# Performance work log

Measured on AMD Instinct MI355X. Metric: run time of the kernel, lower is better.

Reference implementation:

```python
import jax, jax.numpy as jnp
import numpy as np

DT = 0.001
TAU_MEM = 0.01
TAU_SYN = 0.005
THRESHOLD = 1.0
INITIAL_STATE = 0.0
SS_BETA = 100.0  # SuperSpike surrogate slope (Zenke & Ganguli)


@jax.custom_vjp
def superspike(x):
    # Heaviside spike in forward
    return (x > 0).astype(x.dtype)

def _ss_fwd(x):
    return superspike(x), x

def _ss_bwd(x, g):
    # fast-sigmoid surrogate gradient
    return (g / (SS_BETA * jnp.abs(x) + 1.0) ** 2,)

superspike.defvjp(_ss_fwd, _ss_bwd)


def setup_inputs() -> dict:
    key = jax.random.key(0)
    k1, k2 = jax.random.split(key)
    B, T, IN, OUT = 64, 1024, 256, 256
    inputs = jax.random.normal(k1, (B, T, IN), dtype=jnp.float32)
    w = jax.random.normal(k2, (IN, OUT), dtype=jnp.float32) * 4.0  # scale=4.0 in __init__
    return {"inputs": inputs, "w": w}


def _simulate_mem(inputs, w):
    # inputs: [B, T, IN], w: [IN, OUT]
    x = jnp.matmul(inputs, w)  # [B, T, OUT]
    T = x.shape[1]
    dcy_mem = jnp.exp(jnp.asarray(-DT / (TAU_MEM + 1e-16), dtype=x.dtype))
    scl_mem = 1.0 - dcy_mem
    dcy_syn = jnp.exp(jnp.asarray(-DT / (TAU_SYN + 1e-16), dtype=x.dtype))

    zeros0 = jnp.zeros_like(x[:, 0])  # initial_state = 0

    def step(carry, x_t):
        syn, mem = carry
        new_syn = dcy_syn * syn + x_t
        new_mem = dcy_mem * mem + scl_mem * syn  # uses OLD syn
        out = superspike(mem - THRESHOLD)        # spike from OLD mem
        new_mem = new_mem * (1.0 - out)          # reset
        return (new_syn, new_mem), new_mem

    # loop runs over t = 0 .. T-2 (matches `for t in range(nb_steps - 1)`)
    xs = jnp.swapaxes(x[:, : T - 1], 0, 1)  # [T-1, B, OUT]
    _, mems = jax.lax.scan(step, (zeros0, zeros0), xs)
    mems = jnp.swapaxes(mems, 0, 1)  # [B, T-1, OUT]
    # prepend the initial stored state (zeros, since initial_state=0)
    U = jnp.concatenate([zeros0[:, None, :], mems], axis=1)  # [B, T, OUT]
    return U


def reference(inputs, w):
    # monitor == 'mem' -> return membrane potential trace U
    return _simulate_mem(inputs, w)
```

## Files before the change

kernel.cpp:

```cpp
#include <hip/hip_runtime.h>
#include <cmath>

typedef short bf16x8 __attribute__((ext_vector_type(8)));
typedef float f32x4 __attribute__((ext_vector_type(4)));
typedef unsigned short us8v __attribute__((ext_vector_type(8)));

#define T_DIM 1024

__device__ __forceinline__ unsigned short rtn_bf16(float f) {
    unsigned u = __float_as_uint(f);
    return (unsigned short)((u + 0x7FFFu + ((u >> 16) & 1u)) >> 16);
}
__device__ __forceinline__ float bf_to_f(unsigned short h) {
    return __uint_as_float(((unsigned)h) << 16);
}
__device__ __forceinline__ void split3(float f, unsigned short& h1,
                                       unsigned short& h2, unsigned short& h3) {
    unsigned u = __float_as_uint(f);
    h1 = (unsigned short)(u >> 16);
    float r1 = f - __uint_as_float(u & 0xFFFF0000u);
    unsigned u1 = __float_as_uint(r1);
    h2 = (unsigned short)(u1 >> 16);
    float r2 = r1 - __uint_as_float(u1 & 0xFFFF0000u);
    h3 = rtn_bf16(r2);
}

__device__ __forceinline__ void split_store8(const float4& a, const float4& b,
                                             unsigned short* __restrict__ A0,
                                             unsigned short* __restrict__ A1,
                                             unsigned short* __restrict__ A2,
                                             int off) {
    const float fv[8] = {a.x, a.y, a.z, a.w, b.x, b.y, b.z, b.w};
    us8v o1, o2, o3;
    #pragma unroll
    for (int i = 0; i < 8; ++i) {
        unsigned short h1, h2, h3;
        split3(fv[i], h1, h2, h3);
        o1[i] = h1; o2[i] = h2; o3[i] = h3;
    }
    *(us8v*)&A0[off] = o1;
    *(us8v*)&A1[off] = o2;
    *(us8v*)&A2[off] = o3;
}

__global__ __launch_bounds__(256) void lif_wsplit(const float* __restrict__ w,
                                                  unsigned short* __restrict__ wT1,
                                                  unsigned short* __restrict__ wT2,
                                                  unsigned short* __restrict__ wT3) {
    const int id = blockIdx.x * 256 + threadIdx.x;
    const int k = id >> 8, n = id & 255;
    unsigned short h1, h2, h3;
    split3(w[id], h1, h2, h3);
    const int o = n * 256 + k;
    wT1[o] = h1; wT2[o] = h2; wT3[o] = h3;
}

__global__ __launch_bounds__(256) void lif_gemm_mfma(const float* __restrict__ in,
                                                     const unsigned short* __restrict__ wT1,
                                                     const unsigned short* __restrict__ wT2,
                                                     const unsigned short* __restrict__ wT3,
                                                     float* __restrict__ xbuf) {
    __shared__ unsigned short As[2][3][128 * 32];

    const int tid  = threadIdx.x;
    const int bm   = blockIdx.x;
    const int bn   = blockIdx.y;
    const int wave = tid >> 6;
    const int lane = tid & 63;
    const int l15  = lane & 15;
    const int quad = lane >> 4;
    const int wm   = (wave >> 1) * 64;
    const int wn   = (wave & 1) * 64;

    f32x4 acc[4][4];
    #pragma unroll
    for (int i = 0; i < 4; ++i)
        #pragma unroll
        for (int j = 0; j < 4; ++j) acc[i][j] = (f32x4){0.f, 0.f, 0.f, 0.f};

    const int r  = tid >> 1;
    const int hf = tid & 1;
    const int rx = r & 3;
    const int off0 = r * 32 + (((hf << 1) | 0) ^ rx) * 8;
    const int off1 = r * 32 + (((hf << 1) | 1) ^ rx) * 8;
    const float* arow = in + (size_t)(bm * 128 + r) * 256 + hf * 16;

    float4 av0[4];
    #pragma unroll
    for (int j = 0; j < 4; ++j) av0[j] = *(const float4*)(arow + j * 4);
    float4 avn[4];
    #pragma unroll
    for (int j = 0; j < 4; ++j) avn[j] = *(const float4*)(arow + 32 + j * 4);
    split_store8(av0[0], av0[1], &As[0][0][0], &As[0][1][0], &As[0][2][0], off0);
    split_store8(av0[2], av0[3], &As[0][0][0], &As[0][1][0], &As[0][2][0], off1);
    __syncthreads();

    #pragma unroll
    for (int kt = 0; kt < 8; ++kt) {
        const int cur = kt & 1;

        bf16x8 af[3][4];
        #pragma unroll
        for (int mt = 0; mt < 4; ++mt) {
            const int m  = wm + mt * 16 + l15;
            const int ro = m * 32 + ((quad ^ (m & 3)) * 8);
            af[0][mt] = *(const bf16x8*)&As[cur][0][ro];
            af[1][mt] = *(const bf16x8*)&As[cur][1][ro];
            af[2][mt] = *(const bf16x8*)&As[cur][2][ro];
        }

        if (kt < 7) {
            split_store8(avn[0], avn[1], &As[cur ^ 1][0][0], &As[cur ^ 1][1][0],
                         &As[cur ^ 1][2][0], off0);
            split_store8(avn[2], avn[3], &As[cur ^ 1][0][0], &As[cur ^ 1][1][0],
                         &As[cur ^ 1][2][0], off1);
        }

        __syncthreads();

        if (kt < 6) {
            const float* ap = arow + (kt + 2) * 32;
            #pragma unroll
            for (int j = 0; j < 4; ++j) avn[j] = *(const float4*)(ap + j * 4);
        }

        const int k0 = kt * 32;
        size_t wo = (size_t)(bn * 128 + wn + l15) * 256 + k0 + quad * 8;
        bf16x8 b1 = *(const bf16x8*)(wT1 + wo);
        bf16x8 b2 = *(const bf16x8*)(wT2 + wo);
        bf16x8 b3 = *(const bf16x8*)(wT3 + wo);

        #pragma unroll
        for (int nt = 0; nt < 4; ++nt) {
            bf16x8 n1, n2, n3;
            if (nt < 3) {
                const size_t won = wo + (size_t)16 * 256;
                n1 = *(const bf16x8*)(wT1 + won);
                n2 = *(const bf16x8*)(wT2 + won);
                n3 = *(const bf16x8*)(wT3 + won);
            }
            #pragma unroll
            for (int mt = 0; mt < 4; ++mt) {
                f32x4 a = acc[mt][nt];
                a = __builtin_amdgcn_mfma_f32_16x16x32_bf16(af[0][mt], b1, a, 0, 0, 0);
                a = __builtin_amdgcn_mfma_f32_16x16x32_bf16(af[0][mt], b2, a, 0, 0, 0);
                a = __builtin_amdgcn_mfma_f32_16x16x32_bf16(af[1][mt], b1, a, 0, 0, 0);
                a = __builtin_amdgcn_mfma_f32_16x16x32_bf16(af[1][mt], b2, a, 0, 0, 0);
                a = __builtin_amdgcn_mfma_f32_16x16x32_bf16(af[0][mt], b3, a, 0, 0, 0);
                a = __builtin_amdgcn_mfma_f32_16x16x32_bf16(af[2][mt], b1, a, 0, 0, 0);
                acc[mt][nt] = a;
            }
            if (nt < 3) { b1 = n1; b2 = n2; b3 = n3; wo += (size_t)16 * 256; }
        }
    }

    #pragma unroll
    for (int mt = 0; mt < 4; ++mt) {
        #pragma unroll
        for (int nt = 0; nt < 4; ++nt) {
            const int C  = bn * 128 + wn + nt * 16 + l15;
            const int Rb = bm * 128 + wm + mt * 16 + quad * 4;
            #pragma unroll
            for (int reg = 0; reg < 4; ++reg)
                xbuf[(size_t)(Rb + reg) * 256 + C] = acc[mt][nt][reg];
        }
    }
}

__global__ __launch_bounds__(64, 1) void lif_scan(const float* __restrict__ xbuf,
                                                  float* __restrict__ U,
                                                  double dcy_syn, double dcy_mem,
                                                  double scl_mem) {
    const int b = blockIdx.x >> 2;
    const int o = (blockIdx.x & 3) * 64 + threadIdx.x;

    const float* xp = xbuf + (size_t)b * T_DIM * 256 + o;
    float* up = U + (size_t)b * T_DIM * 256 + o;

    up[0] = 0.0f;
    double syn = 0.0, mem = 0.0;

    float bufA[64], bufB[64];
    #pragma unroll
    for (int j = 0; j < 64; ++j)
        bufA[j] = __builtin_nontemporal_load(xp + (size_t)j * 256);

    #pragma unroll 1
    for (int bt = 0; bt < 8; ++bt) {
        const int tb = bt * 128;
        {
            const float* np = xp + (size_t)(tb + 64) * 256;
            #pragma unroll
            for (int j = 0; j < 64; ++j)
                bufB[j] = __builtin_nontemporal_load(np + (size_t)j * 256);
        }
        #pragma unroll
        for (int j = 0; j < 64; ++j) {
            const int t = tb + j;
            double nm = dcy_mem * mem + scl_mem * syn;
            if (mem - 1.0 > 0.0) nm = 0.0;
            syn = dcy_syn * syn + (double)bufA[j];
            mem = nm;
            __builtin_nontemporal_store((float)mem, up + (size_t)(t + 1) * 256);
        }
        if (bt < 7) {
            const float* np = xp + (size_t)(tb + 128) * 256;
            #pragma unroll
            for (int j = 0; j < 64; ++j)
                bufA[j] = __builtin_nontemporal_load(np + (size_t)j * 256);
        }
        #pragma unroll
        for (int j = 0; j < 64; ++j) {
            const int t = tb + 64 + j;
            double nm = dcy_mem * mem + scl_mem * syn;
            if (mem - 1.0 > 0.0) nm = 0.0;
            syn = dcy_syn * syn + (double)bufB[j];
            mem = nm;
            if (t < T_DIM - 1)
                __builtin_nontemporal_store((float)mem, up + (size_t)(t + 1) * 256);
        }
    }
}

extern "C" void kernel_launch(void* const* d_in, const int* in_sizes, int n_in,
                              void* d_out, int out_size, void* d_ws, size_t ws_size,
                              hipStream_t stream) {
    const float* in = (const float*)d_in[0];
    const float* w  = (const float*)d_in[1];
    float* U = (float*)d_out;

    const double dcy_mem = exp(-0.001 / (0.01  + 1e-16));
    const double dcy_syn = exp(-0.001 / (0.005 + 1e-16));
    const double scl_mem = 1.0 - dcy_mem;

    char* ws = (char*)d_ws;
    unsigned short* wT1 = (unsigned short*)ws;
    unsigned short* wT2 = (unsigned short*)(ws + 131072);
    unsigned short* wT3 = (unsigned short*)(ws + 262144);
    float* xbuf = (float*)(ws + 524288);

    lif_wsplit<<<dim3(256), dim3(256), 0, stream>>>(w, wT1, wT2, wT3);
    lif_gemm_mfma<<<dim3(512, 2), dim3(256), 0, stream>>>(in, wT1, wT2, wT3, xbuf);
    lif_scan<<<dim3(256), dim3(64), 0, stream>>>(xbuf, U, dcy_syn, dcy_mem, scl_mem);
}
```

Before: 189.6 us.

## Interleave LDS staging and B prefetch across MFMA loop; plain loads in scan

The GEMM main loop now spreads the split-and-store of the next A tile and the global prefetch across the inner nt iterations, so they overlap with MFMA work. The first B fragment of the next k-tile is prefetched at the end of the current one, and there is one barrier per k-step, at its end. Launch bounds now ask for 3 blocks per CU, which caps registers. The scan kernel switches its xbuf reads from nontemporal to ordinary loads, which may allow cache hits on data the GEMM just wrote. The tighter register cap risks spills.

New measurement: 226.2 us. 19.3% more time.

```diff
diff --git a/kernel.cpp b/kernel.cpp
--- a/kernel.cpp
+++ b/kernel.cpp
@@ -55,11 +55,11 @@
     wT1[o] = h1; wT2[o] = h2; wT3[o] = h3;
 }
 
-__global__ __launch_bounds__(256) void lif_gemm_mfma(const float* __restrict__ in,
-                                                     const unsigned short* __restrict__ wT1,
-                                                     const unsigned short* __restrict__ wT2,
-                                                     const unsigned short* __restrict__ wT3,
-                                                     float* __restrict__ xbuf) {
+__global__ __launch_bounds__(256, 3) void lif_gemm_mfma(const float* __restrict__ in,
+                                                        const unsigned short* __restrict__ wT1,
+                                                        const unsigned short* __restrict__ wT2,
+                                                        const unsigned short* __restrict__ wT3,
+                                                        float* __restrict__ xbuf) {
     __shared__ unsigned short As[2][3][128 * 32];
 
     const int tid  = threadIdx.x;
@@ -85,6 +85,8 @@
     const int off1 = r * 32 + (((hf << 1) | 1) ^ rx) * 8;
     const float* arow = in + (size_t)(bm * 128 + r) * 256 + hf * 16;
 
+    const size_t wrow = (size_t)(bn * 128 + wn + l15) * 256 + quad * 8;
+
     float4 av0[4];
     #pragma unroll
     for (int j = 0; j < 4; ++j) av0[j] = *(const float4*)(arow + j * 4);
@@ -94,6 +96,10 @@
     split_store8(av0[0], av0[1], &As[0][0][0], &As[0][1][0], &As[0][2][0], off0);
     split_store8(av0[2], av0[3], &As[0][0][0], &As[0][1][0], &As[0][2][0], off1);
     __syncthreads();
+
+    bf16x8 b1 = *(const bf16x8*)(wT1 + wrow);
+    bf16x8 b2 = *(const bf16x8*)(wT2 + wrow);
+    bf16x8 b3 = *(const bf16x8*)(wT3 + wrow);
 
     #pragma unroll
     for (int kt = 0; kt < 8; ++kt) {
@@ -109,32 +115,13 @@
             af[2][mt] = *(const bf16x8*)&As[cur][2][ro];
         }
 
-        if (kt < 7) {
-            split_store8(avn[0], avn[1], &As[cur ^ 1][0][0], &As[cur ^ 1][1][0],
-                         &As[cur ^ 1][2][0], off0);
-            split_store8(avn[2], avn[3], &As[cur ^ 1][0][0], &As[cur ^ 1][1][0],
-                         &As[cur ^ 1][2][0], off1);
-        }
-
-        __syncthreads();
-
-        if (kt < 6) {
-            const float* ap = arow + (kt + 2) * 32;
-            #pragma unroll
-            for (int j = 0; j < 4; ++j) avn[j] = *(const float4*)(ap + j * 4);
-        }
-
-        const int k0 = kt * 32;
-        size_t wo = (size_t)(bn * 128 + wn + l15) * 256 + k0 + quad * 8;
-        bf16x8 b1 = *(const bf16x8*)(wT1 + wo);
-        bf16x8 b2 = *(const bf16x8*)(wT2 + wo);
-        bf16x8 b3 = *(const bf16x8*)(wT3 + wo);
-
         #pragma unroll
         for (int nt = 0; nt < 4; ++nt) {
             bf16x8 n1, n2, n3;
-            if (nt < 3) {
-                const size_t won = wo + (size_t)16 * 256;
+            const bool havenext = (nt < 3) || (kt < 7);
+            if (havenext) {
+                const size_t won = (nt < 3) ? (wrow + (size_t)(kt * 32 + (nt + 1) * 4096))
+                                            : (wrow + (size_t)((kt + 1) * 32));
                 n1 = *(const bf16x8*)(wT1 + won);
                 n2 = *(const bf16x8*)(wT2 + won);
                 n3 = *(const bf16x8*)(wT3 + won);
@@ -150,8 +137,21 @@
                 a = __builtin_amdgcn_mfma_f32_16x16x32_bf16(af[2][mt], b1, a, 0, 0, 0);
                 acc[mt][nt] = a;
             }
-            if (nt < 3) { b1 = n1; b2 = n2; b3 = n3; wo += (size_t)16 * 256; }
-        }
+            if (nt == 0 && kt < 7)
+                split_store8(avn[0], avn[1], &As[cur ^ 1][0][0], &As[cur ^ 1][1][0],
+                             &As[cur ^ 1][2][0], off0);
+            if (nt == 1 && kt < 7)
+                split_store8(avn[2], avn[3], &As[cur ^ 1][0][0], &As[cur ^ 1][1][0],
+                             &As[cur ^ 1][2][0], off1);
+            if (nt == 2 && kt < 6) {
+                const float* ap = arow + (kt + 2) * 32;
+                #pragma unroll
+                for (int j = 0; j < 4; ++j) avn[j] = *(const float4*)(ap + j * 4);
+            }
+            if (havenext) { b1 = n1; b2 = n2; b3 = n3; }
+        }
+
+        __syncthreads();
     }
 
     #pragma unroll
@@ -183,7 +183,7 @@
     float bufA[64], bufB[64];
     #pragma unroll
     for (int j = 0; j < 64; ++j)
-        bufA[j] = __builtin_nontemporal_load(xp + (size_t)j * 256);
+        bufA[j] = xp[(size_t)j * 256];
 
     #pragma unroll 1
     for (int bt = 0; bt < 8; ++bt) {
@@ -192,7 +192,7 @@
             const float* np = xp + (size_t)(tb + 64) * 256;
             #pragma unroll
             for (int j = 0; j < 64; ++j)
-                bufB[j] = __builtin_nontemporal_load(np + (size_t)j * 256);
+                bufB[j] = np[(size_t)j * 256];
         }
         #pragma unroll
         for (int j = 0; j < 64; ++j) {
@@ -207,7 +207,7 @@
             const float* np = xp + (size_t)(tb + 128) * 256;
             #pragma unroll
             for (int j = 0; j < 64; ++j)
-                bufA[j] = __builtin_nontemporal_load(np + (size_t)j * 256);
+                bufA[j] = np[(size_t)j * 256];
         }
         #pragma unroll
         for (int j = 0; j < 64; ++j) {
```

## Load GEMM A-operand directly into registers, drop LDS staging and barriers

Applied to the files above, without the earlier changes.

The GEMM kernel no longer stages the split-bf16 A tile through shared memory with double buffering and __syncthreads. Each lane now loads its own fp32 A fragment from global memory in MFMA layout, splits it into three bf16 parts in registers, and prefetches the next k-slice. This removes LDS traffic and barriers, but wave pairs sharing rows now load and split the same A data redundantly, and global loads are less coalesced. The scan kernel also switches its xbuf loads from nontemporal to normal loads so they can hit in cache.

Result: slower. 212.1 us (+11.8%).

```diff
diff --git a/kernel.cpp b/kernel.cpp
--- a/kernel.cpp
+++ b/kernel.cpp
@@ -3,16 +3,12 @@
 
 typedef short bf16x8 __attribute__((ext_vector_type(8)));
 typedef float f32x4 __attribute__((ext_vector_type(4)));
-typedef unsigned short us8v __attribute__((ext_vector_type(8)));
 
 #define T_DIM 1024
 
 __device__ __forceinline__ unsigned short rtn_bf16(float f) {
     unsigned u = __float_as_uint(f);
     return (unsigned short)((u + 0x7FFFu + ((u >> 16) & 1u)) >> 16);
-}
-__device__ __forceinline__ float bf_to_f(unsigned short h) {
-    return __uint_as_float(((unsigned)h) << 16);
 }
 __device__ __forceinline__ void split3(float f, unsigned short& h1,
                                        unsigned short& h2, unsigned short& h3) {
@@ -23,24 +19,6 @@
     h2 = (unsigned short)(u1 >> 16);
     float r2 = r1 - __uint_as_float(u1 & 0xFFFF0000u);
     h3 = rtn_bf16(r2);
-}
-
-__device__ __forceinline__ void split_store8(const float4& a, const float4& b,
-                                             unsigned short* __restrict__ A0,
-                                             unsigned short* __restrict__ A1,
-                                             unsigned short* __restrict__ A2,
-                                             int off) {
-    const float fv[8] = {a.x, a.y, a.z, a.w, b.x, b.y, b.z, b.w};
-    us8v o1, o2, o3;
-    #pragma unroll
-    for (int i = 0; i < 8; ++i) {
-        unsigned short h1, h2, h3;
-        split3(fv[i], h1, h2, h3);
-        o1[i] = h1; o2[i] = h2; o3[i] = h3;
-    }
-    *(us8v*)&A0[off] = o1;
-    *(us8v*)&A1[off] = o2;
-    *(us8v*)&A2[off] = o3;
 }
 
 __global__ __launch_bounds__(256) void lif_wsplit(const float* __restrict__ w,
@@ -60,8 +38,6 @@
                                                      const unsigned short* __restrict__ wT2,
                                                      const unsigned short* __restrict__ wT3,
                                                      float* __restrict__ xbuf) {
-    __shared__ unsigned short As[2][3][128 * 32];
-
     const int tid  = threadIdx.x;
     const int bm   = blockIdx.x;
     const int bn   = blockIdx.y;
@@ -78,57 +54,50 @@
         #pragma unroll
         for (int j = 0; j < 4; ++j) acc[i][j] = (f32x4){0.f, 0.f, 0.f, 0.f};
 
-    const int r  = tid >> 1;
-    const int hf = tid & 1;
-    const int rx = r & 3;
-    const int off0 = r * 32 + (((hf << 1) | 0) ^ rx) * 8;
-    const int off1 = r * 32 + (((hf << 1) | 1) ^ rx) * 8;
-    const float* arow = in + (size_t)(bm * 128 + r) * 256 + hf * 16;
-
-    float4 av0[4];
-    #pragma unroll
-    for (int j = 0; j < 4; ++j) av0[j] = *(const float4*)(arow + j * 4);
-    float4 avn[4];
-    #pragma unroll
-    for (int j = 0; j < 4; ++j) avn[j] = *(const float4*)(arow + 32 + j * 4);
-    split_store8(av0[0], av0[1], &As[0][0][0], &As[0][1][0], &As[0][2][0], off0);
-    split_store8(av0[2], av0[3], &As[0][0][0], &As[0][1][0], &As[0][2][0], off1);
-    __syncthreads();
-
-    #pragma unroll
+    const float* arow0 = in + (size_t)(bm * 128 + wm + l15) * 256 + quad * 8;
+
+    const size_t wrow = (size_t)(bn * 128 + wn + l15) * 256 + quad * 8;
+
+    float4 rv[4][2];
+    #pragma unroll
+    for (int mt = 0; mt < 4; ++mt) {
+        const float* ap = arow0 + mt * 16 * 256;
+        rv[mt][0] = *(const float4*)(ap);
+        rv[mt][1] = *(const float4*)(ap + 4);
+    }
+
+    #pragma unroll 1
     for (int kt = 0; kt < 8; ++kt) {
-        const int cur = kt & 1;
-
-        bf16x8 af[3][4];
-        #pragma unroll
-        for (int mt = 0; mt < 4; ++mt) {
-            const int m  = wm + mt * 16 + l15;
-            const int ro = m * 32 + ((quad ^ (m & 3)) * 8);
-            af[0][mt] = *(const bf16x8*)&As[cur][0][ro];
-            af[1][mt] = *(const bf16x8*)&As[cur][1][ro];
-            af[2][mt] = *(const bf16x8*)&As[cur][2][ro];
-        }
-
-        if (kt < 7) {
-            split_store8(avn[0], avn[1], &As[cur ^ 1][0][0], &As[cur ^ 1][1][0],
-                         &As[cur ^ 1][2][0], off0);
-            split_store8(avn[2], avn[3], &As[cur ^ 1][0][0], &As[cur ^ 1][1][0],
-                         &As[cur ^ 1][2][0], off1);
-        }
-
-        __syncthreads();
-
-        if (kt < 6) {
-            const float* ap = arow + (kt + 2) * 32;
-            #pragma unroll
-            for (int j = 0; j < 4; ++j) avn[j] = *(const float4*)(ap + j * 4);
-        }
-
         const int k0 = kt * 32;
-        size_t wo = (size_t)(bn * 128 + wn + l15) * 256 + k0 + quad * 8;
+
+        size_t wo = wrow + k0;
         bf16x8 b1 = *(const bf16x8*)(wT1 + wo);
         bf16x8 b2 = *(const bf16x8*)(wT2 + wo);
         bf16x8 b3 = *(const bf16x8*)(wT3 + wo);
+
+        bf16x8 af[3][4];
+        #pragma unroll
+        for (int mt = 0; mt < 4; ++mt) {
+            const float fv[8] = {rv[mt][0].x, rv[mt][0].y, rv[mt][0].z, rv[mt][0].w,
+                                 rv[mt][1].x, rv[mt][1].y, rv[mt][1].z, rv[mt][1].w};
+            #pragma unroll
+            for (int i = 0; i < 8; ++i) {
+                unsigned short h1, h2, h3;
+                split3(fv[i], h1, h2, h3);
+                af[0][mt][i] = (short)h1;
+                af[1][mt][i] = (short)h2;
+                af[2][mt][i] = (short)h3;
+            }
+        }
+
+        if (kt < 7) {
+            #pragma unroll
+            for (int mt = 0; mt < 4; ++mt) {
+                const float* ap = arow0 + mt * 16 * 256 + (k0 + 32);
+                rv[mt][0] = *(const float4*)(ap);
+                rv[mt][1] = *(const float4*)(ap + 4);
+            }
+        }
 
         #pragma unroll
         for (int nt = 0; nt < 4; ++nt) {
@@ -183,7 +152,7 @@
     float bufA[64], bufB[64];
     #pragma unroll
     for (int j = 0; j < 64; ++j)
-        bufA[j] = __builtin_nontemporal_load(xp + (size_t)j * 256);
+        bufA[j] = xp[(size_t)j * 256];
 
     #pragma unroll 1
     for (int bt = 0; bt < 8; ++bt) {
@@ -192,7 +161,7 @@
             const float* np = xp + (size_t)(tb + 64) * 256;
             #pragma unroll
             for (int j = 0; j < 64; ++j)
-                bufB[j] = __builtin_nontemporal_load(np + (size_t)j * 256);
+                bufB[j] = np[(size_t)j * 256];
         }
         #pragma unroll
         for (int j = 0; j < 64; ++j) {
@@ -207,7 +176,7 @@
             const float* np = xp + (size_t)(tb + 128) * 256;
             #pragma unroll
             for (int j = 0; j < 64; ++j)
-                bufA[j] = __builtin_nontemporal_load(np + (size_t)j * 256);
+                bufA[j] = np[(size_t)j * 256];
         }
         #pragma unroll
         for (int j = 0; j < 64; ++j) {
```

## Fuse weight split, GEMM and scan into one persistent kernel with grid barriers

Applied to the files above, without the earlier changes.

Merges the three launches (weight split, MFMA GEMM, LIF scan) into a single 512-block kernel that synchronises phases with atomic grid barriers, so each block handles both N tiles of its GEMM row band. This removes two kernel launch gaps and the tail/idle time between dependent kernels. The scan phase uses 64-wide prefetch buffers split into 32-entry halves to fit the 256-thread, 2-blocks-per-CU register budget. It risks deadlock if all 512 blocks are not co-resident, and it adds a memset launch and spin-wait overhead.

After: 345.2 us. 1.82x slower.

```diff
diff --git a/kernel.cpp b/kernel.cpp
--- a/kernel.cpp
+++ b/kernel.cpp
@@ -10,9 +10,6 @@
 __device__ __forceinline__ unsigned short rtn_bf16(float f) {
     unsigned u = __float_as_uint(f);
     return (unsigned short)((u + 0x7FFFu + ((u >> 16) & 1u)) >> 16);
-}
-__device__ __forceinline__ float bf_to_f(unsigned short h) {
-    return __uint_as_float(((unsigned)h) << 16);
 }
 __device__ __forceinline__ void split3(float f, unsigned short& h1,
                                        unsigned short& h2, unsigned short& h3) {
@@ -43,28 +40,27 @@
     *(us8v*)&A2[off] = o3;
 }
 
-__global__ __launch_bounds__(256) void lif_wsplit(const float* __restrict__ w,
-                                                  unsigned short* __restrict__ wT1,
-                                                  unsigned short* __restrict__ wT2,
-                                                  unsigned short* __restrict__ wT3) {
-    const int id = blockIdx.x * 256 + threadIdx.x;
-    const int k = id >> 8, n = id & 255;
-    unsigned short h1, h2, h3;
-    split3(w[id], h1, h2, h3);
-    const int o = n * 256 + k;
-    wT1[o] = h1; wT2[o] = h2; wT3[o] = h3;
-}
-
-__global__ __launch_bounds__(256) void lif_gemm_mfma(const float* __restrict__ in,
-                                                     const unsigned short* __restrict__ wT1,
-                                                     const unsigned short* __restrict__ wT2,
-                                                     const unsigned short* __restrict__ wT3,
-                                                     float* __restrict__ xbuf) {
-    __shared__ unsigned short As[2][3][128 * 32];
-
-    const int tid  = threadIdx.x;
-    const int bm   = blockIdx.x;
-    const int bn   = blockIdx.y;
+__device__ __forceinline__ void grid_bar(unsigned* __restrict__ ctr,
+                                         unsigned target, bool wait) {
+    __syncthreads();
+    if (threadIdx.x == 0) {
+        __hip_atomic_fetch_add(ctr, 1u, __ATOMIC_ACQ_REL, __HIP_MEMORY_SCOPE_AGENT);
+        if (wait) {
+            while (__hip_atomic_load(ctr, __ATOMIC_ACQUIRE,
+                                     __HIP_MEMORY_SCOPE_AGENT) < target)
+                __builtin_amdgcn_s_sleep(4);
+        }
+    }
+    __syncthreads();
+}
+
+__device__ __forceinline__ void gemm_job(const float* __restrict__ in,
+                                         const unsigned short* __restrict__ wT1,
+                                         const unsigned short* __restrict__ wT2,
+                                         const unsigned short* __restrict__ wT3,
+                                         float* __restrict__ xbuf,
+                                         unsigned short (* __restrict__ As)[3][128 * 32],
+                                         int bm, int bn, int tid) {
     const int wave = tid >> 6;
     const int lane = tid & 63;
     const int l15  = lane & 15;
@@ -167,57 +163,85 @@
     }
 }
 
-__global__ __launch_bounds__(64, 1) void lif_scan(const float* __restrict__ xbuf,
+__global__ __launch_bounds__(256, 2) void lif_all(const float* __restrict__ in,
+                                                  const float* __restrict__ w,
+                                                  unsigned short* __restrict__ wT1,
+                                                  unsigned short* __restrict__ wT2,
+                                                  unsigned short* __restrict__ wT3,
+                                                  float* __restrict__ xbuf,
                                                   float* __restrict__ U,
+                                                  unsigned* __restrict__ bars,
                                                   double dcy_syn, double dcy_mem,
                                                   double scl_mem) {
-    const int b = blockIdx.x >> 2;
-    const int o = (blockIdx.x & 3) * 64 + threadIdx.x;
-
-    const float* xp = xbuf + (size_t)b * T_DIM * 256 + o;
-    float* up = U + (size_t)b * T_DIM * 256 + o;
-
-    up[0] = 0.0f;
-    double syn = 0.0, mem = 0.0;
-
-    float bufA[64], bufB[64];
-    #pragma unroll
-    for (int j = 0; j < 64; ++j)
-        bufA[j] = __builtin_nontemporal_load(xp + (size_t)j * 256);
-
-    #pragma unroll 1
-    for (int bt = 0; bt < 8; ++bt) {
-        const int tb = bt * 128;
-        {
-            const float* np = xp + (size_t)(tb + 64) * 256;
-            #pragma unroll
-            for (int j = 0; j < 64; ++j)
-                bufB[j] = __builtin_nontemporal_load(np + (size_t)j * 256);
-        }
-        #pragma unroll
-        for (int j = 0; j < 64; ++j) {
-            const int t = tb + j;
-            double nm = dcy_mem * mem + scl_mem * syn;
-            if (mem - 1.0 > 0.0) nm = 0.0;
-            syn = dcy_syn * syn + (double)bufA[j];
-            mem = nm;
-            __builtin_nontemporal_store((float)mem, up + (size_t)(t + 1) * 256);
-        }
-        if (bt < 7) {
-            const float* np = xp + (size_t)(tb + 128) * 256;
-            #pragma unroll
-            for (int j = 0; j < 64; ++j)
-                bufA[j] = __builtin_nontemporal_load(np + (size_t)j * 256);
-        }
-        #pragma unroll
-        for (int j = 0; j < 64; ++j) {
-            const int t = tb + 64 + j;
-            double nm = dcy_mem * mem + scl_mem * syn;
-            if (mem - 1.0 > 0.0) nm = 0.0;
-            syn = dcy_syn * syn + (double)bufB[j];
-            mem = nm;
-            if (t < T_DIM - 1)
+    __shared__ unsigned short As[2][3][128 * 32];
+
+    const int tid = threadIdx.x;
+    const int blk = blockIdx.x;
+
+    if (blk < 256) {
+        const int gid = blk * 256 + tid;
+        const int k = gid >> 8, n = gid & 255;
+        unsigned short h1, h2, h3;
+        split3(w[gid], h1, h2, h3);
+        const int o = n * 256 + k;
+        wT1[o] = h1; wT2[o] = h2; wT3[o] = h3;
+    }
+    grid_bar(&bars[0], 512, true);
+
+    gemm_job(in, wT1, wT2, wT3, xbuf, As, blk, 0, tid);
+    __syncthreads();
+    gemm_job(in, wT1, wT2, wT3, xbuf, As, blk, 1, tid);
+    grid_bar(&bars[1], 512, blk < 256);
+
+    if (blk < 256 && tid < 64) {
+        const int b = blk >> 2;
+        const int o = (blk & 3) * 64 + tid;
+
+        const float* xp = xbuf + (size_t)b * T_DIM * 256 + o;
+        float* up = U + (size_t)b * T_DIM * 256 + o;
+
+        up[0] = 0.0f;
+        double syn = 0.0, mem = 0.0;
+
+        float bufA[32], bufB[32];
+        #pragma unroll
+        for (int j = 0; j < 32; ++j)
+            bufA[j] = __builtin_nontemporal_load(xp + (size_t)j * 256);
+
+        #pragma unroll 1
+        for (int bt = 0; bt < 16; ++bt) {
+            const int tb = bt * 64;
+            {
+                const float* np = xp + (size_t)(tb + 32) * 256;
+                #pragma unroll
+                for (int j = 0; j < 32; ++j)
+                    bufB[j] = __builtin_nontemporal_load(np + (size_t)j * 256);
+            }
+            #pragma unroll
+            for (int j = 0; j < 32; ++j) {
+                const int t = tb + j;
+                double nm = dcy_mem * mem + scl_mem * syn;
+                if (mem - 1.0 > 0.0) nm = 0.0;
+                syn = dcy_syn * syn + (double)bufA[j];
+                mem = nm;
                 __builtin_nontemporal_store((float)mem, up + (size_t)(t + 1) * 256);
+            }
+            if (bt < 15) {
+                const float* np = xp + (size_t)(tb + 64) * 256;
+                #pragma unroll
+                for (int j = 0; j < 32; ++j)
+                    bufA[j] = __builtin_nontemporal_load(np + (size_t)j * 256);
+            }
+            #pragma unroll
+            for (int j = 0; j < 32; ++j) {
+                const int t = tb + 32 + j;
+                double nm = dcy_mem * mem + scl_mem * syn;
+                if (mem - 1.0 > 0.0) nm = 0.0;
+                syn = dcy_syn * syn + (double)bufB[j];
+                mem = nm;
+                if (t < T_DIM - 1)
+                    __builtin_nontemporal_store((float)mem, up + (size_t)(t + 1) * 256);
+            }
         }
     }
 }
@@ -237,9 +261,10 @@
     unsigned short* wT1 = (unsigned short*)ws;
     unsigned short* wT2 = (unsigned short*)(ws + 131072);
     unsigned short* wT3 = (unsigned short*)(ws + 262144);
+    unsigned* bars      = (unsigned*)(ws + 393216);
     float* xbuf = (float*)(ws + 524288);
 
-    lif_wsplit<<<dim3(256), dim3(256), 0, stream>>>(w, wT1, wT2, wT3);
-    lif_gemm_mfma<<<dim3(512, 2), dim3(256), 0, stream>>>(in, wT1, wT2, wT3, xbuf);
-    lif_scan<<<dim3(256), dim3(64), 0, stream>>>(xbuf, U, dcy_syn, dcy_mem, scl_mem);
-}
+    hipMemsetAsync(bars, 0, 256, stream);
+    lif_all<<<dim3(512), dim3(256), 0, stream>>>(in, w, wT1, wT2, wT3, xbuf, U,
+                                                 bars, dcy_syn, dcy_mem, scl_mem);
+}
```
